# Performance work log

Hardware: AMD Instinct MI355X
Metric: run time of the kernel (lower is better)

Reference implementation:

```python
import jax, jax.numpy as jnp
import numpy as np

N_NODES = 100000
D = 256
B = 2048
U = 8192
R = 8
EPS = 1e-10
AVG_NEIGHBORS = 10.0  # matches num_sample_train=10


def setup_inputs() -> dict:
    key = jax.random.key(0)
    k1, k2, k3, k4, k5, k6 = jax.random.split(key, 6)
    nodes = jax.random.randint(k1, (B,), 0, N_NODES)
    unique_idx = jax.random.randint(k2, (U,), 0, N_NODES)
    # sparse binary relational masks: ~10 sampled neighbors per node per relation
    masks = jax.random.bernoulli(k3, AVG_NEIGHBORS / U, (R, B, U)).astype(jnp.float32)
    embeddings = jax.random.normal(k4, (N_NODES, D), dtype=jnp.float32)
    weight = jax.random.normal(k5, (D, D), dtype=jnp.float32) * (1.0 / np.sqrt(D))
    rel_weights = jax.random.normal(k6, (R, D, D), dtype=jnp.float32) * (1.0 / np.sqrt(D))
    return {"nodes": nodes, "unique_idx": unique_idx, "masks": masks,
            "embeddings": embeddings, "weight": weight, "rel_weights": rel_weights}


def reference(nodes, unique_idx, masks, embeddings, weight, rel_weights):
    # self path: E[nodes] @ W.T  -> [B, D]
    self_out = embeddings[nodes] @ weight.T
    # row-normalize masks by neighbor count (+eps), as in forward_bmm
    norm_masks = masks / (masks.sum(axis=2, keepdims=True) + EPS)  # [R, B, U]
    neigh_emb = embeddings[unique_idx]  # [U, D]
    # per-relation mean aggregation: masks.bmm(neigh_emb) -> [R, B, D]
    agg = jnp.einsum('rbu,ud->rbd', norm_masks, neigh_emb)
    # combine across relations with relation-specific weights and sum: [B, D]
    rel_out = jnp.einsum('rbd,rod->bo', agg, rel_weights)
    return jax.nn.relu(self_out + rel_out)
```

## Files before the change

### kernel.cpp

```cpp
#include <hip/hip_runtime.h>
#include <hip/hip_bf16.h>

constexpr int D      = 256;
constexpr int Bn     = 2048;
constexpr int U      = 8192;
constexpr int R      = 8;
constexpr int KEXT   = R * D + D;
constexpr float EPS  = 1e-10f;
constexpr int CAP    = 256;

typedef __attribute__((ext_vector_type(8))) short bf16x8;
typedef __attribute__((ext_vector_type(4))) float f32x4;
typedef __attribute__((ext_vector_type(4))) unsigned int u32x4;

__global__ __launch_bounds__(256) void build_wt(const float* __restrict__ weight,
                                                const float* __restrict__ relw,
                                                __hip_bfloat16* __restrict__ w2) {
    const int o = blockIdx.x;
    const int t = threadIdx.x;
    #pragma unroll
    for (int c = 0; c < 9; ++c) {
        float v;
        if (c < 8) v = relw[((size_t)(c * D + o)) * D + t];
        else       v = weight[(size_t)o * D + t];
        w2[(size_t)o * KEXT + c * D + t] = __float2bfloat16(v);
    }
}

__global__ __launch_bounds__(256) void scan_agg(const int*   __restrict__ nodes,
                                                const int*   __restrict__ uidx,
                                                const float* __restrict__ masks,
                                                const float* __restrict__ emb,
                                                __hip_bfloat16* __restrict__ A) {
    __shared__ int s_cnt;
    __shared__ int s_u[CAP];
    __shared__ int s_nid[CAP];

    const int tid = threadIdx.x;
    const int bid = blockIdx.x;

    if (bid < R * Bn) {
        if (tid == 0) s_cnt = 0;
        __syncthreads();

        const u32x4* row = (const u32x4*)(masks + (size_t)bid * U);
        unsigned flags = 0u;
        #pragma unroll
        for (int j = 0; j < U / 1024; ++j) {
            u32x4 m = __builtin_nontemporal_load(&row[j * 256 + tid]);
            unsigned f = (m.x ? 1u : 0u) | (m.y ? 2u : 0u) |
                         (m.z ? 4u : 0u) | (m.w ? 8u : 0u);
            flags |= f << (4 * j);
        }

        if (flags) {
            unsigned fl = flags;
            do {
                int bit = __builtin_ctz(fl);
                fl &= fl - 1;
                int j = bit >> 2, c = bit & 3;
                int u = (j * 256 + tid) * 4 + c;
                int p = atomicAdd(&s_cnt, 1);
                if (p < CAP) s_u[p] = u;
            } while (fl);
        }
        __syncthreads();

        const int total = s_cnt;
        const int cnt = total < CAP ? total : CAP;
        if (tid < cnt) s_nid[tid] = uidx[s_u[tid]];
        __syncthreads();

        const float scale = 1.0f / ((float)total + EPS);

        float a0 = 0.f, a1 = 0.f, a2 = 0.f, a3 = 0.f;
        int k = 0;
        for (; k + 4 <= cnt; k += 4) {
            a0 += emb[(size_t)s_nid[k]     * D + tid];
            a1 += emb[(size_t)s_nid[k + 1] * D + tid];
            a2 += emb[(size_t)s_nid[k + 2] * D + tid];
            a3 += emb[(size_t)s_nid[k + 3] * D + tid];
        }
        for (; k < cnt; ++k) a0 += emb[(size_t)s_nid[k] * D + tid];

        const int r = bid >> 11;
        const int b = bid & (Bn - 1);
        A[(size_t)b * KEXT + r * D + tid] =
            __float2bfloat16(((a0 + a1) + (a2 + a3)) * scale);
    } else {
        const int b = bid - R * Bn;
        const int node = nodes[b];
        A[(size_t)b * KEXT + R * D + tid] = __float2bfloat16(emb[(size_t)node * D + tid]);
    }
}

constexpr int SK = 72;

__global__ __launch_bounds__(256) void gemm_mfma(const __hip_bfloat16* __restrict__ A,
                                                 const __hip_bfloat16* __restrict__ W2,
                                                 float* __restrict__ out) {
    __shared__ ushort As[64 * SK];
    __shared__ ushort Bs[64 * SK];

    const int tid  = threadIdx.x;
    const int lane = tid & 63;
    const int wave = tid >> 6;
    const int wm   = wave >> 1;
    const int wn   = wave & 1;
    const int quad = lane >> 4;
    const int rrow = lane & 15;

    const int bn = blockIdx.x * 64;
    const int bm = blockIdx.y * 64;

    const int kq = tid & 7;
    const int m0 = tid >> 3;

    f32x4 acc[2][2];
    #pragma unroll
    for (int i = 0; i < 2; ++i)
        #pragma unroll
        for (int j = 0; j < 2; ++j) acc[i][j] = (f32x4){0.f, 0.f, 0.f, 0.f};

    const ushort* Ag = (const ushort*)A;
    const ushort* Bg = (const ushort*)W2;

    for (int bk = 0; bk < KEXT; bk += 64) {
        *(uint4*)&As[m0 * SK + kq * 8] =
            *(const uint4*)&Ag[(size_t)(bm + m0) * KEXT + bk + kq * 8];
        *(uint4*)&As[(m0 + 32) * SK + kq * 8] =
            *(const uint4*)&Ag[(size_t)(bm + m0 + 32) * KEXT + bk + kq * 8];
        *(uint4*)&Bs[m0 * SK + kq * 8] =
            *(const uint4*)&Bg[(size_t)(bn + m0) * KEXT + bk + kq * 8];
        *(uint4*)&Bs[(m0 + 32) * SK + kq * 8] =
            *(const uint4*)&Bg[(size_t)(bn + m0 + 32) * KEXT + bk + kq * 8];

        __syncthreads();

        #pragma unroll
        for (int kc = 0; kc < 2; ++kc) {
            bf16x8 a0 = *(const bf16x8*)&As[(wm * 32 +  0 + rrow) * SK + kc * 32 + quad * 8];
            bf16x8 a1 = *(const bf16x8*)&As[(wm * 32 + 16 + rrow) * SK + kc * 32 + quad * 8];
            bf16x8 b0 = *(const bf16x8*)&Bs[(wn * 32 +  0 + rrow) * SK + kc * 32 + quad * 8];
            bf16x8 b1 = *(const bf16x8*)&Bs[(wn * 32 + 16 + rrow) * SK + kc * 32 + quad * 8];
            acc[0][0] = __builtin_amdgcn_mfma_f32_16x16x32_bf16(a0, b0, acc[0][0], 0, 0, 0);
            acc[0][1] = __builtin_amdgcn_mfma_f32_16x16x32_bf16(a0, b1, acc[0][1], 0, 0, 0);
            acc[1][0] = __builtin_amdgcn_mfma_f32_16x16x32_bf16(a1, b0, acc[1][0], 0, 0, 0);
            acc[1][1] = __builtin_amdgcn_mfma_f32_16x16x32_bf16(a1, b1, acc[1][1], 0, 0, 0);
        }

        __syncthreads();
    }

    #pragma unroll
    for (int tm = 0; tm < 2; ++tm) {
        #pragma unroll
        for (int tn = 0; tn < 2; ++tn) {
            const int col = bn + wn * 32 + tn * 16 + rrow;
            #pragma unroll
            for (int reg = 0; reg < 4; ++reg) {
                const int row = bm + wm * 32 + tm * 16 + quad * 4 + reg;
                out[(size_t)row * 256 + col] = fmaxf(acc[tm][tn][reg], 0.f);
            }
        }
    }
}

extern "C" void kernel_launch(void* const* d_in, const int* in_sizes, int n_in,
                              void* d_out, int out_size, void* d_ws, size_t ws_size,
                              hipStream_t stream) {
    const int*   nodes  = (const int*)  d_in[0];
    const int*   uidx   = (const int*)  d_in[1];
    const float* masks  = (const float*)d_in[2];
    const float* emb    = (const float*)d_in[3];
    const float* weight = (const float*)d_in[4];
    const float* relw   = (const float*)d_in[5];
    float* out = (float*)d_out;

    __hip_bfloat16* A  = (__hip_bfloat16*)d_ws;
    __hip_bfloat16* W2 = A + (size_t)Bn * KEXT;

    build_wt<<<D, 256, 0, stream>>>(weight, relw, W2);
    scan_agg<<<R * Bn + Bn, 256, 0, stream>>>(nodes, uidx, masks, emb, A);
    gemm_mfma<<<dim3(4, 32), 256, 0, stream>>>(A, W2, out);
}
```

Before: 756.9 us.

## Split mask scan and embedding gather into separate kernels

Splits the fused scan+aggregate kernel into a pure streaming mask-scan kernel that writes per-row neighbor counts and ushort index lists, and a per-node gather kernel that handles all eight relations plus the self embedding. The aim is to keep the bandwidth-bound mask scan free of dependent gather latency, and to gather all of a node's neighbors in one block. The cost is an extra launch and a small round trip through workspace for the lists.

```diff
diff --git a/kernel.cpp b/kernel.cpp
--- a/kernel.cpp
+++ b/kernel.cpp
@@ -27,71 +27,83 @@
     }
 }
 
-__global__ __launch_bounds__(256) void scan_agg(const int*   __restrict__ nodes,
-                                                const int*   __restrict__ uidx,
-                                                const float* __restrict__ masks,
-                                                const float* __restrict__ emb,
-                                                __hip_bfloat16* __restrict__ A) {
+__global__ __launch_bounds__(256) void mask_scan(const float* __restrict__ masks,
+                                                 int* __restrict__ cnts,
+                                                 ushort* __restrict__ lists) {
     __shared__ int s_cnt;
     __shared__ int s_u[CAP];
-    __shared__ int s_nid[CAP];
-
     const int tid = threadIdx.x;
     const int bid = blockIdx.x;
 
-    if (bid < R * Bn) {
-        if (tid == 0) s_cnt = 0;
-        __syncthreads();
-
-        const u32x4* row = (const u32x4*)(masks + (size_t)bid * U);
-        unsigned flags = 0u;
-        #pragma unroll
-        for (int j = 0; j < U / 1024; ++j) {
-            u32x4 m = __builtin_nontemporal_load(&row[j * 256 + tid]);
-            unsigned f = (m.x ? 1u : 0u) | (m.y ? 2u : 0u) |
-                         (m.z ? 4u : 0u) | (m.w ? 8u : 0u);
-            flags |= f << (4 * j);
-        }
-
-        if (flags) {
-            unsigned fl = flags;
-            do {
-                int bit = __builtin_ctz(fl);
-                fl &= fl - 1;
-                int j = bit >> 2, c = bit & 3;
-                int u = (j * 256 + tid) * 4 + c;
-                int p = atomicAdd(&s_cnt, 1);
-                if (p < CAP) s_u[p] = u;
-            } while (fl);
-        }
-        __syncthreads();
-
-        const int total = s_cnt;
-        const int cnt = total < CAP ? total : CAP;
-        if (tid < cnt) s_nid[tid] = uidx[s_u[tid]];
-        __syncthreads();
-
-        const float scale = 1.0f / ((float)total + EPS);
-
+    if (tid == 0) s_cnt = 0;
+    __syncthreads();
+
+    const u32x4* row = (const u32x4*)(masks + (size_t)bid * U);
+    unsigned flags = 0u;
+    #pragma unroll
+    for (int j = 0; j < U / 1024; ++j) {
+        u32x4 m = __builtin_nontemporal_load(&row[j * 256 + tid]);
+        unsigned f = (m.x ? 1u : 0u) | (m.y ? 2u : 0u) |
+                     (m.z ? 4u : 0u) | (m.w ? 8u : 0u);
+        flags |= f << (4 * j);
+    }
+
+    if (flags) {
+        unsigned fl = flags;
+        do {
+            int bit = __builtin_ctz(fl);
+            fl &= fl - 1;
+            int u = ((bit >> 2) * 256 + tid) * 4 + (bit & 3);
+            int p = atomicAdd(&s_cnt, 1);
+            if (p < CAP) s_u[p] = u;
+        } while (fl);
+    }
+    __syncthreads();
+
+    const int total = s_cnt;
+    if (tid == 0) cnts[bid] = total;
+    if (tid < min(total, CAP)) lists[(size_t)bid * CAP + tid] = (ushort)s_u[tid];
+}
+
+__global__ __launch_bounds__(256) void gather_agg(const int* __restrict__ nodes,
+                                                  const int* __restrict__ uidx,
+                                                  const int* __restrict__ cnts,
+                                                  const ushort* __restrict__ lists,
+                                                  const float* __restrict__ emb,
+                                                  __hip_bfloat16* __restrict__ A) {
+    __shared__ int s_nid[R * CAP];
+    __shared__ int s_c[R];
+    const int tid = threadIdx.x;
+    const int b = blockIdx.x;
+
+    if (tid < R) s_c[tid] = cnts[tid * Bn + b];
+    __syncthreads();
+
+    for (int r = 0; r < R; ++r) {
+        int c = min(s_c[r], CAP);
+        if (tid < c)
+            s_nid[r * CAP + tid] = uidx[lists[(size_t)(r * Bn + b) * CAP + tid]];
+    }
+    __syncthreads();
+
+    for (int r = 0; r < R; ++r) {
+        const int c = min(s_c[r], CAP);
+        const int* nid = &s_nid[r * CAP];
         float a0 = 0.f, a1 = 0.f, a2 = 0.f, a3 = 0.f;
         int k = 0;
-        for (; k + 4 <= cnt; k += 4) {
-            a0 += emb[(size_t)s_nid[k]     * D + tid];
-            a1 += emb[(size_t)s_nid[k + 1] * D + tid];
-            a2 += emb[(size_t)s_nid[k + 2] * D + tid];
-            a3 += emb[(size_t)s_nid[k + 3] * D + tid];
+        for (; k + 4 <= c; k += 4) {
+            a0 += emb[(size_t)nid[k]     * D + tid];
+            a1 += emb[(size_t)nid[k + 1] * D + tid];
+            a2 += emb[(size_t)nid[k + 2] * D + tid];
+            a3 += emb[(size_t)nid[k + 3] * D + tid];
         }
-        for (; k < cnt; ++k) a0 += emb[(size_t)s_nid[k] * D + tid];
-
-        const int r = bid >> 11;
-        const int b = bid & (Bn - 1);
+        for (; k < c; ++k) a0 += emb[(size_t)nid[k] * D + tid];
+        const float scale = 1.0f / ((float)s_c[r] + EPS);
         A[(size_t)b * KEXT + r * D + tid] =
             __float2bfloat16(((a0 + a1) + (a2 + a3)) * scale);
-    } else {
-        const int b = bid - R * Bn;
-        const int node = nodes[b];
-        A[(size_t)b * KEXT + R * D + tid] = __float2bfloat16(emb[(size_t)node * D + tid]);
-    }
+    }
+    A[(size_t)b * KEXT + R * D + tid] =
+        __float2bfloat16(emb[(size_t)nodes[b] * D + tid]);
 }
 
 constexpr int SK = 72;
@@ -177,10 +189,13 @@
     const float* relw   = (const float*)d_in[5];
     float* out = (float*)d_out;
 
-    __hip_bfloat16* A  = (__hip_bfloat16*)d_ws;
-    __hip_bfloat16* W2 = A + (size_t)Bn * KEXT;
+    __hip_bfloat16* A     = (__hip_bfloat16*)d_ws;
+    __hip_bfloat16* W2    = A + (size_t)Bn * KEXT;
+    int*            cnts  = (int*)(W2 + (size_t)D * KEXT);
+    ushort*         lists = (ushort*)(cnts + R * Bn);
 
     build_wt<<<D, 256, 0, stream>>>(weight, relw, W2);
-    scan_agg<<<R * Bn + Bn, 256, 0, stream>>>(nodes, uidx, masks, emb, A);
+    mask_scan<<<R * Bn, 256, 0, stream>>>(masks, cnts, lists);
+    gather_agg<<<Bn, 256, 0, stream>>>(nodes, uidx, cnts, lists, emb, A);
     gemm_mfma<<<dim3(4, 32), 256, 0, stream>>>(A, W2, out);
 }
```

Result: no change. 769.6 us (+1.7%).
